# Kernel tuning notes

Measured on AMD Instinct MI355X. Metric: run time of the kernel, lower is better.

## Reference

```python
import jax, jax.numpy as jnp
import numpy as np

P, B, C, H, W = 8, 8, 64, 32, 32


def setup_inputs() -> dict:
    key = jax.random.key(0)
    k1, k2, k3 = jax.random.split(key, 3)
    shape = (P, B, C, H, W)
    return {
        "K_set": jax.random.normal(k1, shape, dtype=jnp.float32),
        "J_set": jax.random.normal(k2, shape, dtype=jnp.float32),
        "V_set": jax.random.normal(k3, shape, dtype=jnp.float32),
    }


def reference(K_set, J_set, V_set):
    # K_set/J_set/V_set: [P, B, C, H, W]; N = H*W spatial tokens.
    p, b, c, h, w = K_set.shape
    n = h * w
    Kf = K_set.reshape(p, b, c, n)  # [P,B,C,N]
    Jf = J_set.reshape(p, b, c, n)  # [P,B,C,N] (original permutes to [B,N,C])
    Vf = V_set.reshape(p, b, c, n)  # [P,B,C,N]
    # scores[p,b,j,k] = sum_c J[p,b,c,j] * K[p,b,c,k]  (unscaled QK^T)
    scores = jnp.einsum('pbcj,pbck->pbjk', Jf, Kf)
    # Original: F.softmax(bmm(J_pie, K_pie), dim=1) -> softmax over the J-token axis (j)
    att = jax.nn.softmax(scores, axis=2)
    # out[p,b,c,k] = sum_j V[p,b,c,j] * att[p,b,j,k]
    out = jnp.einsum('pbcj,pbjk->pbck', Vf, att)
    return out.reshape(p, b, c, h, w)
```

## Files before the change

kernel.cpp:

```cpp
#include <hip/hip_runtime.h>


typedef short bf16x8 __attribute__((ext_vector_type(8)));
typedef short bf16x4 __attribute__((ext_vector_type(4)));
typedef float f32x4  __attribute__((ext_vector_type(4)));

#define NTOK 1024
#define CH   64
#define KTW  128
#define JTILE 32
#define NIT  (NTOK / JTILE)
#define SJK  76
#define SV   36
#define SP   36

__device__ __forceinline__ unsigned short f2bf_rne(float x) {
  unsigned int u = __float_as_uint(x);
  u += 0x7FFFu + ((u >> 16) & 1u);
  return (unsigned short)(u >> 16);
}

#define MFMA(a,b,c) __builtin_amdgcn_mfma_f32_16x16x32_bf16((a),(b),(c),0,0,0)

__global__ __launch_bounds__(256, 2) void attn_v4(
    const float* __restrict__ Kg, const float* __restrict__ Jg,
    const float* __restrict__ Vg, float* __restrict__ Og) {
  __shared__ unsigned short KhS[KTW][SJK];
  __shared__ unsigned short KlS[KTW][SJK];
  __shared__ unsigned short JhS[2][JTILE][SJK];
  __shared__ unsigned short JlS[2][JTILE][SJK];
  __shared__ unsigned short VtS[2][CH][SV];
  __shared__ unsigned short PtS[4][JTILE][SP];

  const int tid  = threadIdx.x;
  const int lane = tid & 63;
  const int wave = tid >> 6;
  const int l15  = lane & 15;
  const int l4   = lane >> 4;

  const int bid   = blockIdx.x;
  const int batch = bid & 63;
  const int ktile = bid >> 6;
  const int k0    = ktile * KTW;
  const size_t base = (size_t)batch * (CH * NTOK);
  const float* Kp = Kg + base;
  const float* Jp = Jg + base;
  const float* Vp = Vg + base;
  float*       Op = Og + base;

  const int jJ   = tid & 31;
  const int octJ = tid >> 5;
  const float* srcJ = Jp + (size_t)(octJ * 8) * NTOK + jJ;
  const int c0  = tid >> 3;
  const int jq0 = tid & 7;
  const float* srcV = Vp + (size_t)c0 * NTOK + jq0 * 4;

  float  jr[8];
  float4 vr[2];

  auto issueJV = [&](int j0) {
    #pragma unroll
    for (int r = 0; r < 8; ++r) jr[r] = srcJ[(size_t)r * NTOK + j0];
    vr[0] = *(const float4*)(srcV + j0);
    vr[1] = *(const float4*)(srcV + (size_t)32 * NTOK + j0);
  };
  auto stageJV = [&](int buf) {
    bf16x8 hv, lv;
    #pragma unroll
    for (int r = 0; r < 8; ++r) {
      unsigned int u = __float_as_uint(jr[r]);
      hv[r] = (short)(u >> 16);
      float hf = __uint_as_float(u & 0xFFFF0000u);
      lv[r] = (short)(__float_as_uint(jr[r] - hf) >> 16);
    }
    *(bf16x8*)&JhS[buf][jJ][octJ * 8] = hv;
    *(bf16x8*)&JlS[buf][jJ][octJ * 8] = lv;
    bf16x4 w0, w1;
    w0[0] = (short)f2bf_rne(vr[0].x); w0[1] = (short)f2bf_rne(vr[0].y);
    w0[2] = (short)f2bf_rne(vr[0].z); w0[3] = (short)f2bf_rne(vr[0].w);
    w1[0] = (short)f2bf_rne(vr[1].x); w1[1] = (short)f2bf_rne(vr[1].y);
    w1[2] = (short)f2bf_rne(vr[1].z); w1[3] = (short)f2bf_rne(vr[1].w);
    *(bf16x4*)&VtS[buf][c0][jq0 * 4]      = w0;
    *(bf16x4*)&VtS[buf][c0 + 32][jq0 * 4] = w1;
  };

  issueJV(0);

  #pragma unroll
  for (int i = 0; i < 4; ++i) {
    int task = i * 256 + tid;
    int k    = task & (KTW - 1);
    int oct  = task >> 7;
    const float* src = Kp + (size_t)(oct * 8) * NTOK + k0 + k;
    bf16x8 hv, lv;
    #pragma unroll
    for (int r = 0; r < 8; ++r) {
      float v = src[(size_t)r * NTOK];
      unsigned int u = __float_as_uint(v);
      hv[r] = (short)(u >> 16);
      float hf = __uint_as_float(u & 0xFFFF0000u);
      lv[r] = (short)(__float_as_uint(v - hf) >> 16);
    }
    *(bf16x8*)&KhS[k][oct * 8] = hv;
    *(bf16x8*)&KlS[k][oct * 8] = lv;
  }
  __syncthreads();

  bf16x8 kbh[2][2], kbl[2][2];
  #pragma unroll
  for (int ks = 0; ks < 2; ++ks)
    #pragma unroll
    for (int cd = 0; cd < 2; ++cd) {
      kbh[ks][cd] = *(const bf16x8*)&KhS[wave * 32 + ks * 16 + l15][cd * 32 + l4 * 8];
      kbl[ks][cd] = *(const bf16x8*)&KlS[wave * 32 + ks * 16 + l15][cd * 32 + l4 * 8];
      asm volatile("" : "+v"(kbh[ks][cd]), "+v"(kbl[ks][cd]));
    }

  stageJV(0);
  __syncthreads();

  f32x4 U[4][2];
  #pragma unroll
  for (int a = 0; a < 4; ++a)
    #pragma unroll
    for (int b = 0; b < 2; ++b) U[a][b] = (f32x4){0.f, 0.f, 0.f, 0.f};
  float zacc0 = 0.f, zacc1 = 0.f;

  int cur = 0;
  #pragma unroll 1
  for (int it = 0; it < NIT; ++it) {
    if (it + 1 < NIT) issueJV((it + 1) * JTILE);

    f32x4 S[2][2];
    #pragma unroll
    for (int a = 0; a < 2; ++a)
      #pragma unroll
      for (int b = 0; b < 2; ++b) S[a][b] = (f32x4){0.f, 0.f, 0.f, 0.f};
    __builtin_amdgcn_s_setprio(1);
    #pragma unroll
    for (int cd = 0; cd < 2; ++cd) {
      const int co = cd * 32 + l4 * 8;
      bf16x8 ah0 = *(const bf16x8*)&JhS[cur][l15][co];
      bf16x8 ah1 = *(const bf16x8*)&JhS[cur][l15 + 16][co];
      bf16x8 al0 = *(const bf16x8*)&JlS[cur][l15][co];
      bf16x8 al1 = *(const bf16x8*)&JlS[cur][l15 + 16][co];
      #pragma unroll
      for (int ks = 0; ks < 2; ++ks) {
        S[0][ks] = MFMA(ah0, kbh[ks][cd], S[0][ks]);
        S[0][ks] = MFMA(ah0, kbl[ks][cd], S[0][ks]);
        S[0][ks] = MFMA(al0, kbh[ks][cd], S[0][ks]);
        S[1][ks] = MFMA(ah1, kbh[ks][cd], S[1][ks]);
        S[1][ks] = MFMA(ah1, kbl[ks][cd], S[1][ks]);
        S[1][ks] = MFMA(al1, kbh[ks][cd], S[1][ks]);
      }
    }
    __builtin_amdgcn_s_setprio(0);

    #pragma unroll
    for (int js = 0; js < 2; ++js)
      #pragma unroll
      for (int ks = 0; ks < 2; ++ks) {
        f32x4 s = S[js][ks];
        float e0 = __expf(s[0]);
        float e1 = __expf(s[1]);
        float e2 = __expf(s[2]);
        float e3 = __expf(s[3]);
        if (ks == 0) zacc0 += (e0 + e1) + (e2 + e3);
        else         zacc1 += (e0 + e1) + (e2 + e3);
        bf16x4 pv;
        pv[0] = (short)f2bf_rne(e0); pv[1] = (short)f2bf_rne(e1);
        pv[2] = (short)f2bf_rne(e2); pv[3] = (short)f2bf_rne(e3);
        *(bf16x4*)&PtS[wave][ks * 16 + l15][js * 16 + l4 * 4] = pv;
      }

    bf16x8 pb0 = *(const bf16x8*)&PtS[wave][l15][l4 * 8];
    bf16x8 pb1 = *(const bf16x8*)&PtS[wave][16 + l15][l4 * 8];
    __builtin_amdgcn_s_setprio(1);
    #pragma unroll
    for (int ct = 0; ct < 4; ++ct) {
      bf16x8 av = *(const bf16x8*)&VtS[cur][ct * 16 + l15][l4 * 8];
      U[ct][0] = MFMA(av, pb0, U[ct][0]);
      U[ct][1] = MFMA(av, pb1, U[ct][1]);
    }
    __builtin_amdgcn_s_setprio(0);

    if (it + 1 < NIT) stageJV(cur ^ 1);
    __syncthreads();
    cur ^= 1;
  }

  float z0 = zacc0; z0 += __shfl_xor(z0, 16); z0 += __shfl_xor(z0, 32);
  float z1 = zacc1; z1 += __shfl_xor(z1, 16); z1 += __shfl_xor(z1, 32);
  const float rz0 = 1.0f / z0;
  const float rz1 = 1.0f / z1;
  const int kbase = k0 + wave * 32;
  #pragma unroll
  for (int ct = 0; ct < 4; ++ct)
    #pragma unroll
    for (int r = 0; r < 4; ++r) {
      int c = ct * 16 + l4 * 4 + r;
      Op[(size_t)c * NTOK + kbase + l15]      = U[ct][0][r] * rz0;
      Op[(size_t)c * NTOK + kbase + 16 + l15] = U[ct][1][r] * rz1;
    }
}

extern "C" void kernel_launch(void* const* d_in, const int* in_sizes, int n_in,
                              void* d_out, int out_size, void* d_ws, size_t ws_size,
                              hipStream_t stream) {
  const float* Kg = (const float*)d_in[0];
  const float* Jg = (const float*)d_in[1];
  const float* Vg = (const float*)d_in[2];
  float* Og = (float*)d_out;
  attn_v4<<<dim3(512), dim3(256), 0, stream>>>(Kg, Jg, Vg, Og);
}
```

Before: 125.7 us.

## Split work across 8 waves per block over j and channel halves; fold log2e into K

Doubles the block to 512 threads. Each of the 8 waves handles a 16-row half of the J tile and a 32-channel half of the output, so each wave issues half the MFMAs and holds fewer registers. This adds a block-wide barrier each iteration before the P·V step, because P is now produced by two waves, and a shared-memory exchange to combine the softmax denominators at the end. K is pre-scaled by log2(e) so exp2f can replace __expf. The extra synchronisation and the 4-blocks-per-CU launch bound trade per-iteration barrier cost for more waves in flight to hide latency.

```diff
diff --git a/kernel.cpp b/kernel.cpp
--- a/kernel.cpp
+++ b/kernel.cpp
@@ -13,6 +13,7 @@
 #define SJK  76
 #define SV   36
 #define SP   36
+#define LOG2E 1.4426950408889634f
 
 __device__ __forceinline__ unsigned short f2bf_rne(float x) {
   unsigned int u = __float_as_uint(x);
@@ -22,7 +23,7 @@
 
 #define MFMA(a,b,c) __builtin_amdgcn_mfma_f32_16x16x32_bf16((a),(b),(c),0,0,0)
 
-__global__ __launch_bounds__(256, 2) void attn_v4(
+__global__ __launch_bounds__(512, 4) void attn_v6(
     const float* __restrict__ Kg, const float* __restrict__ Jg,
     const float* __restrict__ Vg, float* __restrict__ Og) {
   __shared__ unsigned short KhS[KTW][SJK];
@@ -35,6 +36,8 @@
   const int tid  = threadIdx.x;
   const int lane = tid & 63;
   const int wave = tid >> 6;
+  const int wk   = wave & 3;
+  const int wj   = wave >> 2;
   const int l15  = lane & 15;
   const int l4   = lane >> 4;
 
@@ -48,61 +51,65 @@
   const float* Vp = Vg + base;
   float*       Op = Og + base;
 
-  const int jJ   = tid & 31;
-  const int octJ = tid >> 5;
-  const float* srcJ = Jp + (size_t)(octJ * 8) * NTOK + jJ;
+  const int jJ  = tid & 31;
+  const int cq  = tid >> 5;
+  const float* srcJ = Jp + (size_t)(cq * 4) * NTOK + jJ;
   const int c0  = tid >> 3;
   const int jq0 = tid & 7;
   const float* srcV = Vp + (size_t)c0 * NTOK + jq0 * 4;
 
-  float  jr[8];
-  float4 vr[2];
+  float  jr[4];
+  float4 vr;
 
   auto issueJV = [&](int j0) {
     #pragma unroll
-    for (int r = 0; r < 8; ++r) jr[r] = srcJ[(size_t)r * NTOK + j0];
-    vr[0] = *(const float4*)(srcV + j0);
-    vr[1] = *(const float4*)(srcV + (size_t)32 * NTOK + j0);
+    for (int r = 0; r < 4; ++r) jr[r] = srcJ[(size_t)r * NTOK + j0];
+    vr = *(const float4*)(srcV + j0);
   };
   auto stageJV = [&](int buf) {
-    bf16x8 hv, lv;
-    #pragma unroll
-    for (int r = 0; r < 8; ++r) {
+    bf16x4 hv, lv;
+    #pragma unroll
+    for (int r = 0; r < 4; ++r) {
       unsigned int u = __float_as_uint(jr[r]);
       hv[r] = (short)(u >> 16);
       float hf = __uint_as_float(u & 0xFFFF0000u);
       lv[r] = (short)(__float_as_uint(jr[r] - hf) >> 16);
     }
-    *(bf16x8*)&JhS[buf][jJ][octJ * 8] = hv;
-    *(bf16x8*)&JlS[buf][jJ][octJ * 8] = lv;
-    bf16x4 w0, w1;
-    w0[0] = (short)f2bf_rne(vr[0].x); w0[1] = (short)f2bf_rne(vr[0].y);
-    w0[2] = (short)f2bf_rne(vr[0].z); w0[3] = (short)f2bf_rne(vr[0].w);
-    w1[0] = (short)f2bf_rne(vr[1].x); w1[1] = (short)f2bf_rne(vr[1].y);
-    w1[2] = (short)f2bf_rne(vr[1].z); w1[3] = (short)f2bf_rne(vr[1].w);
-    *(bf16x4*)&VtS[buf][c0][jq0 * 4]      = w0;
-    *(bf16x4*)&VtS[buf][c0 + 32][jq0 * 4] = w1;
+    *(bf16x4*)&JhS[buf][jJ][cq * 4] = hv;
+    *(bf16x4*)&JlS[buf][jJ][cq * 4] = lv;
+    bf16x4 w;
+    w[0] = (short)f2bf_rne(vr.x); w[1] = (short)f2bf_rne(vr.y);
+    w[2] = (short)f2bf_rne(vr.z); w[3] = (short)f2bf_rne(vr.w);
+    *(bf16x4*)&VtS[buf][c0][jq0 * 4] = w;
   };
 
   issueJV(0);
 
-  #pragma unroll
-  for (int i = 0; i < 4; ++i) {
-    int task = i * 256 + tid;
-    int k    = task & (KTW - 1);
-    int oct  = task >> 7;
-    const float* src = Kp + (size_t)(oct * 8) * NTOK + k0 + k;
-    bf16x8 hv, lv;
+  {
+    const int kk   = tid & 127;
+    const int oct4 = tid >> 7;
+    const float* srcK = Kp + (size_t)(oct4 * 16) * NTOK + k0 + kk;
+    bf16x8 hv0, lv0, hv1, lv1;
     #pragma unroll
     for (int r = 0; r < 8; ++r) {
-      float v = src[(size_t)r * NTOK];
+      float v = srcK[(size_t)r * NTOK] * LOG2E;
       unsigned int u = __float_as_uint(v);
-      hv[r] = (short)(u >> 16);
+      hv0[r] = (short)(u >> 16);
       float hf = __uint_as_float(u & 0xFFFF0000u);
-      lv[r] = (short)(__float_as_uint(v - hf) >> 16);
-    }
-    *(bf16x8*)&KhS[k][oct * 8] = hv;
-    *(bf16x8*)&KlS[k][oct * 8] = lv;
+      lv0[r] = (short)(__float_as_uint(v - hf) >> 16);
+    }
+    #pragma unroll
+    for (int r = 0; r < 8; ++r) {
+      float v = srcK[(size_t)(8 + r) * NTOK] * LOG2E;
+      unsigned int u = __float_as_uint(v);
+      hv1[r] = (short)(u >> 16);
+      float hf = __uint_as_float(u & 0xFFFF0000u);
+      lv1[r] = (short)(__float_as_uint(v - hf) >> 16);
+    }
+    *(bf16x8*)&KhS[kk][oct4 * 16]     = hv0;
+    *(bf16x8*)&KhS[kk][oct4 * 16 + 8] = hv1;
+    *(bf16x8*)&KlS[kk][oct4 * 16]     = lv0;
+    *(bf16x8*)&KlS[kk][oct4 * 16 + 8] = lv1;
   }
   __syncthreads();
 
@@ -111,17 +118,17 @@
   for (int ks = 0; ks < 2; ++ks)
     #pragma unroll
     for (int cd = 0; cd < 2; ++cd) {
-      kbh[ks][cd] = *(const bf16x8*)&KhS[wave * 32 + ks * 16 + l15][cd * 32 + l4 * 8];
-      kbl[ks][cd] = *(const bf16x8*)&KlS[wave * 32 + ks * 16 + l15][cd * 32 + l4 * 8];
+      kbh[ks][cd] = *(const bf16x8*)&KhS[wk * 32 + ks * 16 + l15][cd * 32 + l4 * 8];
+      kbl[ks][cd] = *(const bf16x8*)&KlS[wk * 32 + ks * 16 + l15][cd * 32 + l4 * 8];
       asm volatile("" : "+v"(kbh[ks][cd]), "+v"(kbl[ks][cd]));
     }
 
   stageJV(0);
   __syncthreads();
 
-  f32x4 U[4][2];
+  f32x4 U[2][2];
   #pragma unroll
-  for (int a = 0; a < 4; ++a)
+  for (int a = 0; a < 2; ++a)
     #pragma unroll
     for (int b = 0; b < 2; ++b) U[a][b] = (f32x4){0.f, 0.f, 0.f, 0.f};
   float zacc0 = 0.f, zacc1 = 0.f;
@@ -131,54 +138,46 @@
   for (int it = 0; it < NIT; ++it) {
     if (it + 1 < NIT) issueJV((it + 1) * JTILE);
 
-    f32x4 S[2][2];
-    #pragma unroll
-    for (int a = 0; a < 2; ++a)
-      #pragma unroll
-      for (int b = 0; b < 2; ++b) S[a][b] = (f32x4){0.f, 0.f, 0.f, 0.f};
+    f32x4 S[2];
+    S[0] = (f32x4){0.f, 0.f, 0.f, 0.f};
+    S[1] = (f32x4){0.f, 0.f, 0.f, 0.f};
     __builtin_amdgcn_s_setprio(1);
     #pragma unroll
     for (int cd = 0; cd < 2; ++cd) {
       const int co = cd * 32 + l4 * 8;
-      bf16x8 ah0 = *(const bf16x8*)&JhS[cur][l15][co];
-      bf16x8 ah1 = *(const bf16x8*)&JhS[cur][l15 + 16][co];
-      bf16x8 al0 = *(const bf16x8*)&JlS[cur][l15][co];
-      bf16x8 al1 = *(const bf16x8*)&JlS[cur][l15 + 16][co];
+      bf16x8 ah = *(const bf16x8*)&JhS[cur][wj * 16 + l15][co];
+      bf16x8 al = *(const bf16x8*)&JlS[cur][wj * 16 + l15][co];
       #pragma unroll
       for (int ks = 0; ks < 2; ++ks) {
-        S[0][ks] = MFMA(ah0, kbh[ks][cd], S[0][ks]);
-        S[0][ks] = MFMA(ah0, kbl[ks][cd], S[0][ks]);
-        S[0][ks] = MFMA(al0, kbh[ks][cd], S[0][ks]);
-        S[1][ks] = MFMA(ah1, kbh[ks][cd], S[1][ks]);
-        S[1][ks] = MFMA(ah1, kbl[ks][cd], S[1][ks]);
-        S[1][ks] = MFMA(al1, kbh[ks][cd], S[1][ks]);
+        S[ks] = MFMA(ah, kbh[ks][cd], S[ks]);
+        S[ks] = MFMA(ah, kbl[ks][cd], S[ks]);
+        S[ks] = MFMA(al, kbh[ks][cd], S[ks]);
       }
     }
     __builtin_amdgcn_s_setprio(0);
 
     #pragma unroll
-    for (int js = 0; js < 2; ++js)
-      #pragma unroll
-      for (int ks = 0; ks < 2; ++ks) {
-        f32x4 s = S[js][ks];
-        float e0 = __expf(s[0]);
-        float e1 = __expf(s[1]);
-        float e2 = __expf(s[2]);
-        float e3 = __expf(s[3]);
-        if (ks == 0) zacc0 += (e0 + e1) + (e2 + e3);
-        else         zacc1 += (e0 + e1) + (e2 + e3);
-        bf16x4 pv;
-        pv[0] = (short)f2bf_rne(e0); pv[1] = (short)f2bf_rne(e1);
-        pv[2] = (short)f2bf_rne(e2); pv[3] = (short)f2bf_rne(e3);
-        *(bf16x4*)&PtS[wave][ks * 16 + l15][js * 16 + l4 * 4] = pv;
-      }
-
-    bf16x8 pb0 = *(const bf16x8*)&PtS[wave][l15][l4 * 8];
-    bf16x8 pb1 = *(const bf16x8*)&PtS[wave][16 + l15][l4 * 8];
+    for (int ks = 0; ks < 2; ++ks) {
+      f32x4 s = S[ks];
+      float e0 = exp2f(s[0]);
+      float e1 = exp2f(s[1]);
+      float e2 = exp2f(s[2]);
+      float e3 = exp2f(s[3]);
+      if (ks == 0) zacc0 += (e0 + e1) + (e2 + e3);
+      else         zacc1 += (e0 + e1) + (e2 + e3);
+      bf16x4 pv;
+      pv[0] = (short)f2bf_rne(e0); pv[1] = (short)f2bf_rne(e1);
+      pv[2] = (short)f2bf_rne(e2); pv[3] = (short)f2bf_rne(e3);
+      *(bf16x4*)&PtS[wk][ks * 16 + l15][wj * 16 + l4 * 4] = pv;
+    }
+    __syncthreads();
+
+    bf16x8 pb0 = *(const bf16x8*)&PtS[wk][l15][l4 * 8];
+    bf16x8 pb1 = *(const bf16x8*)&PtS[wk][16 + l15][l4 * 8];
     __builtin_amdgcn_s_setprio(1);
     #pragma unroll
-    for (int ct = 0; ct < 4; ++ct) {
-      bf16x8 av = *(const bf16x8*)&VtS[cur][ct * 16 + l15][l4 * 8];
+    for (int ct = 0; ct < 2; ++ct) {
+      bf16x8 av = *(const bf16x8*)&VtS[cur][wj * 32 + ct * 16 + l15][l4 * 8];
       U[ct][0] = MFMA(av, pb0, U[ct][0]);
       U[ct][1] = MFMA(av, pb1, U[ct][1]);
     }
@@ -191,14 +190,24 @@
 
   float z0 = zacc0; z0 += __shfl_xor(z0, 16); z0 += __shfl_xor(z0, 32);
   float z1 = zacc1; z1 += __shfl_xor(z1, 16); z1 += __shfl_xor(z1, 32);
+
+  float* ZL = (float*)&PtS[0][0][0];
+  if (lane < 16) {
+    ZL[(wk * 2 + wj) * 32 + l15]      = z0;
+    ZL[(wk * 2 + wj) * 32 + 16 + l15] = z1;
+  }
+  __syncthreads();
+  z0 += ZL[(wk * 2 + (wj ^ 1)) * 32 + l15];
+  z1 += ZL[(wk * 2 + (wj ^ 1)) * 32 + 16 + l15];
   const float rz0 = 1.0f / z0;
   const float rz1 = 1.0f / z1;
-  const int kbase = k0 + wave * 32;
+
+  const int kbase = k0 + wk * 32;
   #pragma unroll
-  for (int ct = 0; ct < 4; ++ct)
+  for (int ct = 0; ct < 2; ++ct)
     #pragma unroll
     for (int r = 0; r < 4; ++r) {
-      int c = ct * 16 + l4 * 4 + r;
+      int c = wj * 32 + ct * 16 + l4 * 4 + r;
       Op[(size_t)c * NTOK + kbase + l15]      = U[ct][0][r] * rz0;
       Op[(size_t)c * NTOK + kbase + 16 + l15] = U[ct][1][r] * rz1;
     }
@@ -211,5 +220,5 @@
   const float* Jg = (const float*)d_in[1];
   const float* Vg = (const float*)d_in[2];
   float* Og = (float*)d_out;
-  attn_v4<<<dim3(512), dim3(256), 0, stream>>>(Kg, Jg, Vg, Og);
+  attn_v6<<<dim3(512), dim3(512), 0, stream>>>(Kg, Jg, Vg, Og);
 }
```

Result: slower. 132.2 us (+5.2%).
